# Kernel tuning notes

Hardware: AMD Instinct MI355X
Metric: run time of the kernel (lower is better)

The kernel has to match this reference:

```python
import jax, jax.numpy as jnp
import numpy as np

N = 50000
E = 625000
D_IN = 128
D_OUT = 128
NEG_SLOPE = 0.01  # torch LeakyReLU default


def setup_inputs() -> dict:
    key = jax.random.key(0)
    k1, k2, k3, k4, k5, k6, k7, k8 = jax.random.split(key, 8)
    features = jax.random.normal(k1, (N, D_IN), dtype=jnp.float32)
    target = jax.random.randint(k2, (E,), 0, N, dtype=jnp.int64)
    neighbor = jax.random.randint(k3, (E,), 0, N, dtype=jnp.int64)
    values = jax.random.uniform(k4, (E,), dtype=jnp.float32)
    # nn.Linear params (kaiming-uniform-ish init: U(-1/sqrt(in), 1/sqrt(in)))
    bound = 1.0 / np.sqrt(D_IN)
    W1 = jax.random.uniform(k5, (D_OUT, D_IN), minval=-bound, maxval=bound, dtype=jnp.float32)
    b1 = jax.random.uniform(k6, (D_OUT,), minval=-bound, maxval=bound, dtype=jnp.float32)
    W2 = jax.random.uniform(k7, (D_OUT, D_IN), minval=-bound, maxval=bound, dtype=jnp.float32)
    b2 = jax.random.uniform(k8, (D_OUT,), minval=-bound, maxval=bound, dtype=jnp.float32)
    return {"features": features, "target": target, "neighbor": neighbor,
            "values": values, "W1": W1, "b1": b1, "W2": W2, "b2": b2}


def reference(features, target, neighbor, values, W1, b1, W2, b2):
    # gather-scale: msg[e] = features[neighbor[e]] * values[e]
    msg = features[neighbor] * values[:, None]              # (E, D_IN)
    # scatter-add into target nodes
    h_neigh = jax.ops.segment_sum(msg, target, num_segments=N)  # (N, D_IN)
    # dual linear fusion + leaky relu
    h = (features + h_neigh) @ W1.T + b1 + (features * h_neigh) @ W2.T + b2
    return jnp.where(h >= 0, h, NEG_SLOPE * h)
```

## Files before the change

### kernel.cpp

```cpp
#include <hip/hip_runtime.h>

#define D 128
#define CAP 40
#define NEG_SLOPE 0.01f

typedef float v4f __attribute__((ext_vector_type(4)));
typedef short short8 __attribute__((ext_vector_type(8)));

static __device__ __forceinline__ short f2bf(float f) {
    unsigned u = __float_as_uint(f);
    unsigned r = (u + 0x7fffu + ((u >> 16) & 1u)) >> 16;
    return (short)r;
}
static __device__ __forceinline__ float bflo(unsigned u) { return __uint_as_float(u << 16); }
static __device__ __forceinline__ float bfhi(unsigned u) { return __uint_as_float(u & 0xffff0000u); }
static __device__ __forceinline__ unsigned packbf(float x, float y) {
    return (unsigned)(unsigned short)f2bf(x) | ((unsigned)(unsigned short)f2bf(y) << 16);
}

__global__ __launch_bounds__(256) void conv_kernel(const float* __restrict__ feat,
                                                   const float* __restrict__ W1,
                                                   const float* __restrict__ W2,
                                                   unsigned* __restrict__ featbf,
                                                   short* __restrict__ Wbf, int nPairs) {
    int i = blockIdx.x * 256 + threadIdx.x;
    if (i < nPairs) {
        float2 f = ((const float2*)feat)[i];
        featbf[i] = packbf(f.x, f.y);
    }
    if (i < D * D) {
        Wbf[i]         = f2bf(W1[i]);
        Wbf[D * D + i] = f2bf(W2[i]);
    }
}

__global__ __launch_bounds__(256) void bucket_kernel(const int* __restrict__ tgt,
                                                     const int* __restrict__ nbr,
                                                     const float* __restrict__ vals,
                                                     int* __restrict__ deg,
                                                     int2* __restrict__ edata, int E) {
    int e = blockIdx.x * 256 + threadIdx.x;
    if (e >= E) return;
    int t    = tgt[e];
    int slot = atomicAdd(&deg[t], 1);
    if (slot < CAP) {
        int2 ed;
        ed.x = nbr[e];
        ed.y = __float_as_int(vals[e]);
        edata[(long)t * CAP + slot] = ed;
    }
}

__global__ __launch_bounds__(256) void gather_kernel(const unsigned* __restrict__ featbf,
                                                     const int2* __restrict__ edata,
                                                     const int* __restrict__ deg,
                                                     const int* __restrict__ tgt,
                                                     const int* __restrict__ nbr,
                                                     const float* __restrict__ vals,
                                                     unsigned* __restrict__ X1,
                                                     unsigned* __restrict__ X2,
                                                     int nNodes, int E) {
    int wid  = (blockIdx.x * 256 + threadIdx.x) >> 6;
    int lane = threadIdx.x & 63;
    if (wid >= nNodes) return;
    int d = deg[wid];
    float accx = 0.f, accy = 0.f;

    if (d <= CAP) {
        const int2* ep = edata + (long)wid * CAP;
        int j = 0;
        for (; j + 4 <= d; j += 4) {
            int2 e0 = ep[j + 0], e1 = ep[j + 1], e2 = ep[j + 2], e3 = ep[j + 3];
            unsigned u0 = featbf[(long)e0.x * (D / 2) + lane];
            unsigned u1 = featbf[(long)e1.x * (D / 2) + lane];
            unsigned u2 = featbf[(long)e2.x * (D / 2) + lane];
            unsigned u3 = featbf[(long)e3.x * (D / 2) + lane];
            float v0 = __int_as_float(e0.y), v1 = __int_as_float(e1.y);
            float v2 = __int_as_float(e2.y), v3 = __int_as_float(e3.y);
            accx += bflo(u0) * v0; accy += bfhi(u0) * v0;
            accx += bflo(u1) * v1; accy += bfhi(u1) * v1;
            accx += bflo(u2) * v2; accy += bfhi(u2) * v2;
            accx += bflo(u3) * v3; accy += bfhi(u3) * v3;
        }
        for (; j < d; j++) {
            int2 e0 = ep[j];
            unsigned u0 = featbf[(long)e0.x * (D / 2) + lane];
            float v0 = __int_as_float(e0.y);
            accx += bflo(u0) * v0;
            accy += bfhi(u0) * v0;
        }
    } else {
        for (int base = 0; base < E; base += 64) {
            int e = base + lane;
            int t = (e < E) ? tgt[e] : -1;
            unsigned long long m = __ballot(t == wid);
            while (m) {
                int b = __ffsll((long long)m) - 1;
                m &= m - 1;
                int   ee = base + b;
                int   nb = nbr[ee];
                float v  = vals[ee];
                unsigned u = featbf[(long)nb * (D / 2) + lane];
                accx += bflo(u) * v;
                accy += bfhi(u) * v;
            }
        }
    }

    unsigned uf = featbf[(long)wid * (D / 2) + lane];
    float fx = bflo(uf), fy = bfhi(uf);
    X1[(long)wid * (D / 2) + lane] = packbf(fx + accx, fy + accy);
    X2[(long)wid * (D / 2) + lane] = packbf(fx * accx, fy * accy);
}

__global__ __launch_bounds__(256) void gemm_kernel(const short* __restrict__ X1s,
                                                   const short* __restrict__ X2s,
                                                   const short* __restrict__ Wbf,
                                                   const float* __restrict__ b1,
                                                   const float* __restrict__ b2,
                                                   float* __restrict__ out, int nNodes) {
    __shared__ __align__(16) short sW[2 * D * D];

    int tid = threadIdx.x;
    for (int c = tid; c < 4096; c += 256) {
        int r  = c >> 4;
        int cc = c & 15;
        int pp = cc ^ (r & 15);
        *(short8*)(&sW[r * D + pp * 8]) = *(const short8*)(Wbf + c * 8);
    }
    __syncthreads();

    int lane = tid & 63;
    int wid  = (blockIdx.x * 256 + tid) >> 6;
    int m0   = wid * 32;
    if (m0 >= nNodes) return;
    bool t2 = (m0 + 16) < nNodes;

    int mrow = lane & 15;
    int quad = lane >> 4;

    const short* xa1 = X1s + (long)(m0 + mrow) * D + quad * 8;
    const short* xa2 = X2s + (long)(m0 + mrow) * D + quad * 8;
    const short* xb1 = xa1 + 16 * D;
    const short* xb2 = xa2 + 16 * D;

    v4f acc[2][8];
#pragma unroll
    for (int t = 0; t < 2; t++)
#pragma unroll
        for (int i = 0; i < 8; i++) acc[t][i] = (v4f)(0.0f);

#pragma unroll
    for (int s = 0; s < 4; s++) {
        short8 a1 = *(const short8*)(xa1 + s * 32);
        short8 a2 = *(const short8*)(xa2 + s * 32);
        short8 c1, c2;
        if (t2) {
            c1 = *(const short8*)(xb1 + s * 32);
            c2 = *(const short8*)(xb2 + s * 32);
        }
        int pp = (s * 4 + quad) ^ mrow;
#pragma unroll
        for (int ot = 0; ot < 8; ot++) {
            int row = ot * 16 + mrow;
            short8 w1 = *(const short8*)(&sW[row * D + pp * 8]);
            short8 w2 = *(const short8*)(&sW[D * D + row * D + pp * 8]);
            acc[0][ot] = __builtin_amdgcn_mfma_f32_16x16x32_bf16(a1, w1, acc[0][ot], 0, 0, 0);
            acc[0][ot] = __builtin_amdgcn_mfma_f32_16x16x32_bf16(a2, w2, acc[0][ot], 0, 0, 0);
            if (t2) {
                acc[1][ot] = __builtin_amdgcn_mfma_f32_16x16x32_bf16(c1, w1, acc[1][ot], 0, 0, 0);
                acc[1][ot] = __builtin_amdgcn_mfma_f32_16x16x32_bf16(c2, w2, acc[1][ot], 0, 0, 0);
            }
        }
    }

#pragma unroll
    for (int ot = 0; ot < 8; ot++) {
        int   o    = ot * 16 + mrow;
        float bias = b1[o] + b2[o];
#pragma unroll
        for (int r = 0; r < 4; r++) {
            int   node = m0 + quad * 4 + r;
            float v    = acc[0][ot][r] + bias;
            out[(long)node * D + o] = (v >= 0.0f) ? v : NEG_SLOPE * v;
            if (t2) {
                float w = acc[1][ot][r] + bias;
                out[(long)(node + 16) * D + o] = (w >= 0.0f) ? w : NEG_SLOPE * w;
            }
        }
    }
}

extern "C" void kernel_launch(void* const* d_in, const int* in_sizes, int n_in,
                              void* d_out, int out_size, void* d_ws, size_t ws_size,
                              hipStream_t stream) {
    const float* feat = (const float*)d_in[0];
    const int*   tgt  = (const int*)d_in[1];
    const int*   nbr  = (const int*)d_in[2];
    const float* vals = (const float*)d_in[3];
    const float* W1   = (const float*)d_in[4];
    const float* b1   = (const float*)d_in[5];
    const float* W2   = (const float*)d_in[6];
    const float* b2   = (const float*)d_in[7];
    float*       out  = (float*)d_out;

    int E      = in_sizes[1];
    int nNodes = out_size / D;

    int*      deg    = (int*)d_ws;
    int2*     edata  = (int2*)(deg + nNodes);
    short*    Wbf    = (short*)(edata + (long)nNodes * CAP);
    unsigned* featbf = (unsigned*)(Wbf + 2 * D * D);
    unsigned* X1     = featbf + (long)nNodes * (D / 2);
    unsigned* X2     = X1 + (long)nNodes * (D / 2);

    int nPairs = nNodes * (D / 2);

    hipMemsetAsync(deg, 0, (size_t)nNodes * sizeof(int), stream);
    conv_kernel<<<(nPairs + 255) / 256, 256, 0, stream>>>(feat, W1, W2, featbf, Wbf, nPairs);
    bucket_kernel<<<(E + 255) / 256, 256, 0, stream>>>(tgt, nbr, vals, deg, edata, E);
    gather_kernel<<<(nNodes * 64 + 255) / 256, 256, 0, stream>>>(featbf, edata, deg, tgt, nbr, vals,
                                                                 X1, X2, nNodes, E);

    int nPairTiles = (nNodes + 31) / 32;
    int nBlocks    = (nPairTiles + 3) / 4;
    gemm_kernel<<<nBlocks, 256, 0, stream>>>((const short*)X1, (const short*)X2, Wbf, b1, b2, out, nNodes);
}
```

Measured before the change: 182.9 us.

## Fuse conversion and bucketing kernels; split wave halves across edges in gather

```diff
diff --git a/kernel.cpp b/kernel.cpp
--- a/kernel.cpp
+++ b/kernel.cpp
@@ -18,11 +18,17 @@
     return (unsigned)(unsigned short)f2bf(x) | ((unsigned)(unsigned short)f2bf(y) << 16);
 }
 
-__global__ __launch_bounds__(256) void conv_kernel(const float* __restrict__ feat,
-                                                   const float* __restrict__ W1,
-                                                   const float* __restrict__ W2,
-                                                   unsigned* __restrict__ featbf,
-                                                   short* __restrict__ Wbf, int nPairs) {
+__global__ __launch_bounds__(256) void convbucket_kernel(const float* __restrict__ feat,
+                                                         const float* __restrict__ W1,
+                                                         const float* __restrict__ W2,
+                                                         const int* __restrict__ tgt,
+                                                         const int* __restrict__ nbr,
+                                                         const float* __restrict__ vals,
+                                                         unsigned* __restrict__ featbf,
+                                                         short* __restrict__ Wbf,
+                                                         int* __restrict__ deg,
+                                                         int2* __restrict__ edata,
+                                                         int nPairs, int E) {
     int i = blockIdx.x * 256 + threadIdx.x;
     if (i < nPairs) {
         float2 f = ((const float2*)feat)[i];
@@ -32,22 +38,15 @@
         Wbf[i]         = f2bf(W1[i]);
         Wbf[D * D + i] = f2bf(W2[i]);
     }
-}
-
-__global__ __launch_bounds__(256) void bucket_kernel(const int* __restrict__ tgt,
-                                                     const int* __restrict__ nbr,
-                                                     const float* __restrict__ vals,
-                                                     int* __restrict__ deg,
-                                                     int2* __restrict__ edata, int E) {
-    int e = blockIdx.x * 256 + threadIdx.x;
-    if (e >= E) return;
-    int t    = tgt[e];
-    int slot = atomicAdd(&deg[t], 1);
-    if (slot < CAP) {
-        int2 ed;
-        ed.x = nbr[e];
-        ed.y = __float_as_int(vals[e]);
-        edata[(long)t * CAP + slot] = ed;
+    if (i < E) {
+        int t    = tgt[i];
+        int slot = atomicAdd(&deg[t], 1);
+        if (slot < CAP) {
+            int2 ed;
+            ed.x = nbr[i];
+            ed.y = __float_as_int(vals[i]);
+            edata[(long)t * CAP + slot] = ed;
+        }
     }
 }
 
@@ -62,32 +61,41 @@
                                                      int nNodes, int E) {
     int wid  = (blockIdx.x * 256 + threadIdx.x) >> 6;
     int lane = threadIdx.x & 63;
+    int half = lane >> 5;
+    int hl   = lane & 31;
     if (wid >= nNodes) return;
     int d = deg[wid];
-    float accx = 0.f, accy = 0.f;
+
+    const uint2* feat2 = (const uint2*)featbf;
+
+    float a0 = 0.f, a1 = 0.f, a2 = 0.f, a3 = 0.f;
+    float c0 = 0.f, c1 = 0.f, c2 = 0.f, c3 = 0.f;
 
     if (d <= CAP) {
         const int2* ep = edata + (long)wid * CAP;
         int j = 0;
-        for (; j + 4 <= d; j += 4) {
-            int2 e0 = ep[j + 0], e1 = ep[j + 1], e2 = ep[j + 2], e3 = ep[j + 3];
-            unsigned u0 = featbf[(long)e0.x * (D / 2) + lane];
-            unsigned u1 = featbf[(long)e1.x * (D / 2) + lane];
-            unsigned u2 = featbf[(long)e2.x * (D / 2) + lane];
-            unsigned u3 = featbf[(long)e3.x * (D / 2) + lane];
-            float v0 = __int_as_float(e0.y), v1 = __int_as_float(e1.y);
-            float v2 = __int_as_float(e2.y), v3 = __int_as_float(e3.y);
-            accx += bflo(u0) * v0; accy += bfhi(u0) * v0;
-            accx += bflo(u1) * v1; accy += bfhi(u1) * v1;
-            accx += bflo(u2) * v2; accy += bfhi(u2) * v2;
-            accx += bflo(u3) * v3; accy += bfhi(u3) * v3;
-        }
-        for (; j < d; j++) {
-            int2 e0 = ep[j];
-            unsigned u0 = featbf[(long)e0.x * (D / 2) + lane];
-            float v0 = __int_as_float(e0.y);
-            accx += bflo(u0) * v0;
-            accy += bfhi(u0) * v0;
+        for (; j + 8 <= d; j += 8) {
+            int2 p0 = ep[j + half];
+            int2 p1 = ep[j + 2 + half];
+            int2 p2 = ep[j + 4 + half];
+            int2 p3 = ep[j + 6 + half];
+            uint2 u0 = feat2[(long)p0.x * 32 + hl];
+            uint2 u1 = feat2[(long)p1.x * 32 + hl];
+            uint2 u2 = feat2[(long)p2.x * 32 + hl];
+            uint2 u3 = feat2[(long)p3.x * 32 + hl];
+            float v0 = __int_as_float(p0.y), v1 = __int_as_float(p1.y);
+            float v2 = __int_as_float(p2.y), v3 = __int_as_float(p3.y);
+            a0 += bflo(u0.x) * v0; a1 += bfhi(u0.x) * v0; a2 += bflo(u0.y) * v0; a3 += bfhi(u0.y) * v0;
+            c0 += bflo(u1.x) * v1; c1 += bfhi(u1.x) * v1; c2 += bflo(u1.y) * v1; c3 += bfhi(u1.y) * v1;
+            a0 += bflo(u2.x) * v2; a1 += bfhi(u2.x) * v2; a2 += bflo(u2.y) * v2; a3 += bfhi(u2.y) * v2;
+            c0 += bflo(u3.x) * v3; c1 += bfhi(u3.x) * v3; c2 += bflo(u3.y) * v3; c3 += bfhi(u3.y) * v3;
+        }
+        for (; j < d; j += 2) {
+            int   idx = j + half;
+            int2  p   = ep[(idx < d) ? idx : j];
+            float v   = (idx < d) ? __int_as_float(p.y) : 0.0f;
+            uint2 u   = feat2[(long)p.x * 32 + hl];
+            a0 += bflo(u.x) * v; a1 += bfhi(u.x) * v; a2 += bflo(u.y) * v; a3 += bfhi(u.y) * v;
         }
     } else {
         for (int base = 0; base < E; base += 64) {
@@ -100,17 +108,30 @@
                 int   ee = base + b;
                 int   nb = nbr[ee];
                 float v  = vals[ee];
-                unsigned u = featbf[(long)nb * (D / 2) + lane];
-                accx += bflo(u) * v;
-                accy += bfhi(u) * v;
+                if (half == 0) {
+                    uint2 u = feat2[(long)nb * 32 + hl];
+                    a0 += bflo(u.x) * v; a1 += bfhi(u.x) * v;
+                    a2 += bflo(u.y) * v; a3 += bfhi(u.y) * v;
+                }
             }
         }
     }
 
-    unsigned uf = featbf[(long)wid * (D / 2) + lane];
-    float fx = bflo(uf), fy = bfhi(uf);
-    X1[(long)wid * (D / 2) + lane] = packbf(fx + accx, fy + accy);
-    X2[(long)wid * (D / 2) + lane] = packbf(fx * accx, fy * accy);
+    a0 += c0; a1 += c1; a2 += c2; a3 += c3;
+    a0 += __shfl_xor(a0, 32);
+    a1 += __shfl_xor(a1, 32);
+    a2 += __shfl_xor(a2, 32);
+    a3 += __shfl_xor(a3, 32);
+
+    if (half == 0) {
+        uint2 uf = feat2[(long)wid * 32 + hl];
+        float f0 = bflo(uf.x), f1 = bfhi(uf.x), f2 = bflo(uf.y), f3 = bfhi(uf.y);
+        uint2 o1, o2;
+        o1.x = packbf(f0 + a0, f1 + a1); o1.y = packbf(f2 + a2, f3 + a3);
+        o2.x = packbf(f0 * a0, f1 * a1); o2.y = packbf(f2 * a2, f3 * a3);
+        ((uint2*)X1)[(long)wid * 32 + hl] = o1;
+        ((uint2*)X2)[(long)wid * 32 + hl] = o2;
+    }
 }
 
 __global__ __launch_bounds__(256) void gemm_kernel(const short* __restrict__ X1s,
@@ -217,8 +238,8 @@
     int nPairs = nNodes * (D / 2);
 
     hipMemsetAsync(deg, 0, (size_t)nNodes * sizeof(int), stream);
-    conv_kernel<<<(nPairs + 255) / 256, 256, 0, stream>>>(feat, W1, W2, featbf, Wbf, nPairs);
-    bucket_kernel<<<(E + 255) / 256, 256, 0, stream>>>(tgt, nbr, vals, deg, edata, E);
+    convbucket_kernel<<<(nPairs + 255) / 256, 256, 0, stream>>>(feat, W1, W2, tgt, nbr, vals,
+                                                                featbf, Wbf, deg, edata, nPairs, E);
     gather_kernel<<<(nNodes * 64 + 255) / 256, 256, 0, stream>>>(featbf, edata, deg, tgt, nbr, vals,
                                                                  X1, X2, nNodes, E);
 
```

After: 180.1 us. No clear change (-1.5%).
